# Kernel tuning notes

Measured on AMD Instinct MI355X. Metric: run time of the kernel, lower is better.

Reference implementation:

```python
import jax, jax.numpy as jnp
import numpy as np

P = 8          # patch_size
DIM = 256      # embed dim
HEADS = 8
HEAD_DIM = DIM // HEADS
CH = 3
PATCH_DIM = CH * P * P  # 192
INNER = int(4.0 * DIM)  # 1024
SCALE = HEAD_DIM ** -0.5


def sine_pos_embedding(n, c, dtype=jnp.float32):
    # standard 1D sinusoidal position encoding, shape (n, c)
    pos = jnp.arange(n, dtype=jnp.float32)[:, None]            # (n,1)
    div = jnp.exp(jnp.arange(0, c, 2, dtype=jnp.float32) * (-np.log(10000.0) / c))
    pe = jnp.zeros((n, c), dtype=jnp.float32)
    pe = pe.at[:, 0::2].set(jnp.sin(pos * div))
    pe = pe.at[:, 1::2].set(jnp.cos(pos * div))
    return pe.astype(dtype)


def patchify(x):
    # (B,C,H,W) -> (B, n, p1*p2*C), matching 'b c (h p1) (w p2) -> b (h w) (p1 p2 c)'
    B, C, H, W = x.shape
    hp, wp = H // P, W // P
    x = x.reshape(B, C, hp, P, wp, P)
    x = x.transpose(0, 2, 4, 3, 5, 1)        # (B, hp, wp, p1, p2, C)
    return x.reshape(B, hp * wp, P * P * C)


def unpatchify(x, hp, wp):
    # (B, n, p1*p2*C) -> (B, C, H, W)
    B = x.shape[0]
    x = x.reshape(B, hp, wp, P, P, CH)
    x = x.transpose(0, 5, 1, 3, 2, 4)        # (B, C, hp, p1, wp, p2)
    return x.reshape(B, CH, hp * P, wp * P)


def setup_inputs() -> dict:
    key = jax.random.key(0)
    ks = jax.random.split(key, 16)
    B, H, W = 8, 256, 256
    s = 0.02
    img0 = jax.random.normal(ks[0], (B, CH, H, W), dtype=jnp.float32)
    img1 = jax.random.normal(ks[1], (B, CH, H, W), dtype=jnp.float32)
    mask = jax.random.randint(ks[2], (B, 1, H, W), 0, 2).astype(jnp.float32)
    return {
        "img0": img0,
        "img1": img1,
        "mask": mask,
        "w_patch": jax.random.normal(ks[3], (PATCH_DIM, DIM), jnp.float32) * s,
        "b_patch": jnp.zeros((DIM,), jnp.float32),
        "w_kv": jax.random.normal(ks[4], (DIM, 2 * DIM), jnp.float32) * s,
        "b_kv": jnp.zeros((2 * DIM,), jnp.float32),
        "w_qv": jax.random.normal(ks[5], (DIM, 2 * DIM), jnp.float32) * s,
        "b_qv": jnp.zeros((2 * DIM,), jnp.float32),
        "w_fc1": jax.random.normal(ks[6], (DIM, INNER), jnp.float32) * s,
        "b_fc1": jnp.zeros((INNER,), jnp.float32),
        "w_fc2": jax.random.normal(ks[7], (INNER, PATCH_DIM), jnp.float32) * s,
        "b_fc2": jnp.zeros((PATCH_DIM,), jnp.float32),
    }


def reference(img0, img1, mask, w_patch, b_patch, w_kv, b_kv, w_qv, b_qv,
              w_fc1, b_fc1, w_fc2, b_fc2):
    B, C, H, W = img0.shape
    hp, wp = H // P, W // P
    n = hp * wp

    x0 = patchify(img0) @ w_patch + b_patch   # (B, n, dim)
    x1 = patchify(img1) @ w_patch + b_patch
    pe = sine_pos_embedding(n, DIM)
    x0 = x0 + pe
    x1 = x1 + pe

    # img0 -> k, v
    kv = (x0 @ w_kv + b_kv).reshape(B, n, 2, HEADS, HEAD_DIM)
    kv = kv.transpose(2, 0, 3, 1, 4)          # (2, B, heads, n, hd)
    k, v = kv[0], kv[1]

    # img1 -> q (v1 unused in forward, matching torch code)
    qv = (x1 @ w_qv + b_qv).reshape(B, n, 2, DIM).transpose(2, 0, 1, 3)
    q = qv[0].reshape(B, n, HEADS, HEAD_DIM).transpose(0, 2, 1, 3)  # (B, heads, n, hd)

    dots = jnp.einsum('bhqd,bhkd->bhqk', q, k) * SCALE  # (B, heads, n, n)

    # mask: (B,1,H,W) -> per-patch sum -> binary -> additive bias over key dim
    msum = mask.reshape(B, 1, hp, P, wp, P).sum(axis=(3, 5)).reshape(B, 1, n)
    bias = jnp.where(msum > 0, 0.0, -100.0)[:, :, None, :]  # (B,1,1,n)

    attn = jax.nn.softmax(dots + bias, axis=-1)
    out = jnp.einsum('bhqk,bhkd->bhqd', attn, v)
    out = out.transpose(0, 2, 1, 3).reshape(B, n, DIM)

    # mlp2: Linear -> GELU(exact) -> Linear
    h = jax.nn.gelu(out @ w_fc1 + b_fc1, approximate=False)
    res = h @ w_fc2 + b_fc2                   # (B, n, patch_dim)

    return unpatchify(res, hp, wp)            # (B, C, H, W)
```

## Files before the change

### kernel.cpp

```cpp
#include <hip/hip_runtime.h>
#include <cstdint>
#include <cstddef>

typedef __bf16 bf16_t;
typedef uint32_t u32;
typedef __bf16 bf16x4 __attribute__((ext_vector_type(4)));
typedef __bf16 bf16x8 __attribute__((ext_vector_type(8)));
typedef float f32x4 __attribute__((ext_vector_type(4)));
typedef float f32x16 __attribute__((ext_vector_type(16)));

__device__ __forceinline__ void gload_lds16(const bf16_t* g, bf16_t* l) {
  __builtin_amdgcn_global_load_lds((const __attribute__((address_space(1))) void*)g,
                                   (__attribute__((address_space(3))) void*)l,
                                   16, 0, 0);
}

__device__ __forceinline__ f32x4 mfma16(bf16x8 a, bf16x8 b, f32x4 c) {
  return __builtin_amdgcn_mfma_f32_16x16x32_bf16(a, b, c, 0, 0, 0);
}
__device__ __forceinline__ f32x16 mfma32(bf16x8 a, bf16x8 b, f32x16 c) {
  return __builtin_amdgcn_mfma_f32_32x32x16_bf16(a, b, c, 0, 0, 0);
}

#define LOG2E 1.4426950408889634f

__global__ __launch_bounds__(256)
void prep_all(const float* __restrict__ img0, const float* __restrict__ img1,
              const float* __restrict__ mask,
              const float* __restrict__ wp, const float* __restrict__ wkv,
              const float* __restrict__ wqv, const float* __restrict__ wfc1,
              const float* __restrict__ wfc2,
              bf16_t* __restrict__ xp0, bf16_t* __restrict__ xp1,
              float* __restrict__ pe, float* __restrict__ bias,
              bf16_t* __restrict__ wpT, bf16_t* __restrict__ wkvT,
              bf16_t* __restrict__ wqT, bf16_t* __restrict__ wfc1T,
              bf16_t* __restrict__ wfc2T) {
  __shared__ float tl[64 * 65];
  int bid = blockIdx.x, tid = threadIdx.x;
  if (bid < 1536) {
    int imgsel = bid >= 768;
    int t = (bid - (imgsel ? 768 : 0)) * 256 + tid;
    const float* img = imgsel ? img1 : img0;
    bf16_t* xp = imgsel ? xp1 : xp0;
    int wpp = t & 31, p1 = (t >> 5) & 7, hp = (t >> 8) & 31, rest = t >> 13;
    int b = rest / 3, c = rest - b * 3;
    const float* src = img + (((size_t)(b * 3 + c) * 256 + hp * 8 + p1) * 256 + wpp * 8);
    float4 v0 = *(const float4*)src;
    float4 v1 = *(const float4*)(src + 4);
    int row = b * 1024 + hp * 32 + wpp;
    bf16_t* dst = xp + (size_t)row * 192 + p1 * 24 + c;
    dst[0]  = (bf16_t)v0.x; dst[3]  = (bf16_t)v0.y; dst[6]  = (bf16_t)v0.z; dst[9]  = (bf16_t)v0.w;
    dst[12] = (bf16_t)v1.x; dst[15] = (bf16_t)v1.y; dst[18] = (bf16_t)v1.z; dst[21] = (bf16_t)v1.w;
  } else if (bid < 2560) {
    int t = bid - 1536, c = tid;
    int i2 = c & ~1;
    float div = __expf((float)i2 * (-9.210340371976184f / 256.0f));
    float arg = (float)t * div;
    float sv, cv;
    __sincosf(arg, &sv, &cv);
    pe[t * 256 + c] = (c & 1) ? cv : sv;
  } else if (bid < 2592) {
    int g = (bid - 2560) * 256 + tid;
    int b = g >> 10, t = g & 1023, hp = t >> 5, wpp = t & 31;
    const float* mp = mask + ((size_t)b * 256 + hp * 8) * 256 + wpp * 8;
    float s = 0.f;
    #pragma unroll
    for (int p1 = 0; p1 < 8; p1++) {
      float4 a = *(const float4*)(mp + p1 * 256);
      float4 c = *(const float4*)(mp + p1 * 256 + 4);
      s += a.x + a.y + a.z + a.w + c.x + c.y + c.z + c.w;
    }
    bias[g] = (s > 0.f) ? 0.f : (-100.f * LOG2E);
  } else {
    int i = bid - 2592;
    const float* src; bf16_t* dst; int srcN, dstK, NT;
    if (i >= 172) {
      int j = i - 172;
      bf16_t* p = wfc2T + 192 * 1024 + j * 8192 + tid * 32;
      bf16x8 z;
      #pragma unroll
      for (int e = 0; e < 8; e++) z[e] = (bf16_t)0.0f;
      *(bf16x8*)(p) = z; *(bf16x8*)(p + 8) = z;
      *(bf16x8*)(p + 16) = z; *(bf16x8*)(p + 24) = z;
      return;
    }
    if (i < 12)       { src = wp;   dst = wpT;   srcN = 256;  dstK = 192;  NT = 4; }
    else if (i < 44)  { i -= 12;  src = wkv;  dst = wkvT;  srcN = 512;  dstK = 256;  NT = 8; }
    else if (i < 60)  { i -= 44;  src = wqv;  dst = wqT;   srcN = 512;  dstK = 256;  NT = 4; }
    else if (i < 124) { i -= 60;  src = wfc1; dst = wfc1T; srcN = 1024; dstK = 256;  NT = 16; }
    else              { i -= 124; src = wfc2; dst = wfc2T; srcN = 192;  dstK = 1024; NT = 3; }
    int kt = i / NT, nt = i - kt * NT;
    #pragma unroll
    for (int j = 0; j < 4; j++) {
      int r = (tid >> 4) + 16 * j, c = (tid & 15) * 4;
      float4 v = *(const float4*)(src + (size_t)(kt * 64 + r) * srcN + nt * 64 + c);
      tl[r * 65 + c] = v.x; tl[r * 65 + c + 1] = v.y;
      tl[r * 65 + c + 2] = v.z; tl[r * 65 + c + 3] = v.w;
    }
    __syncthreads();
    #pragma unroll
    for (int j = 0; j < 16; j++) {
      int flat = tid + 256 * j;
      int n_l = flat >> 6, k_l = flat & 63;
      dst[(size_t)(nt * 64 + n_l) * dstK + kt * 64 + k_l] = (bf16_t)tl[k_l * 65 + n_l];
    }
  }
}

template<int EPI, int BN>
__global__ __launch_bounds__(256)
void gemm_bt(const bf16_t* __restrict__ A_, const bf16_t* __restrict__ A2,
             const bf16_t* __restrict__ Bt_, const bf16_t* __restrict__ Bt2,
             int M, int N, int K,
             const float* __restrict__ bias_, const float* __restrict__ bias2,
             const float* __restrict__ pe,
             bf16_t* __restrict__ out_b, bf16_t* __restrict__ out_b2,
             bf16_t* __restrict__ out_b3, float* __restrict__ out_f) {
  constexpr int NF = BN / 32;
  __shared__ bf16_t alds[2][8 * 64 * 8];
  __shared__ bf16_t blds[2][8 * BN * 8];
  const int tid = threadIdx.x;
  const int lane = tid & 63, wid = tid >> 6;
  const int ln15 = lane & 15, hi = lane >> 4;
  const int brow = blockIdx.x * 64;
  int bcol = blockIdx.y * BN;
  const bf16_t* A = A_;
  const bf16_t* Bt = Bt_;
  const float* bias = bias_;
  bool qpart = false;
  if (EPI == 0 && blockIdx.z) A = A2;
  if (EPI == 5 && blockIdx.y >= 4) {
    qpart = true; A = A2; Bt = Bt2; bias = bias2; bcol -= 512;
  }
  const int wr = wid >> 1, wc = wid & 1;

  auto stage = [&](int buf, int k0) {
    #pragma unroll
    for (int s = 0; s < 2; s++) {
      int c = tid + s * 256; int kb = c >> 6, row = c & 63;
      gload_lds16(A + (size_t)(brow + row) * K + k0 + kb * 8,
                  &alds[buf][(size_t)(s * 256 + wid * 64) * 8]);
    }
    #pragma unroll
    for (int s = 0; s < BN / 32; s++) {
      int c = tid + s * 256; int kb = c / BN, row = c & (BN - 1);
      gload_lds16(Bt + (size_t)(bcol + row) * K + k0 + kb * 8,
                  &blds[buf][(size_t)(s * 256 + wid * 64) * 8]);
    }
  };

  f32x4 acc[2][NF];
  #pragma unroll
  for (int m = 0; m < 2; m++)
    #pragma unroll
    for (int n = 0; n < NF; n++) acc[m][n] = (f32x4){0.f, 0.f, 0.f, 0.f};

  stage(0, 0);
  __syncthreads();
  int cur = 0;
  const int NT = K >> 6;
  for (int t = 0; t < NT; t++) {
    if (t + 1 < NT) stage(cur ^ 1, (t + 1) << 6);
    bf16x8 af[2][2], bfr[2][NF];
    #pragma unroll
    for (int kk = 0; kk < 2; kk++) {
      #pragma unroll
      for (int m = 0; m < 2; m++)
        af[kk][m] = *(const bf16x8*)&alds[cur][(size_t)((kk * 4 + hi) * 64 + wr * 32 + m * 16 + ln15) * 8];
      #pragma unroll
      for (int n = 0; n < NF; n++)
        bfr[kk][n] = *(const bf16x8*)&blds[cur][(size_t)((kk * 4 + hi) * BN + wc * (BN / 2) + n * 16 + ln15) * 8];
    }
    #pragma unroll
    for (int kk = 0; kk < 2; kk++)
      #pragma unroll
      for (int m = 0; m < 2; m++)
        #pragma unroll
        for (int n = 0; n < NF; n++)
          acc[m][n] = mfma16(af[kk][m], bfr[kk][n], acc[m][n]);
    __syncthreads();
    cur ^= 1;
  }

  #pragma unroll
  for (int m = 0; m < 2; m++) {
    #pragma unroll
    for (int n = 0; n < NF; n++) {
      #pragma unroll
      for (int r = 0; r < 4; r++) {
        int grow = brow + wr * 32 + m * 16 + hi * 4 + r;
        int gcol = bcol + wc * (BN / 2) + n * 16 + ln15;
        float v = acc[m][n][r];
        if (EPI == 0) {
          v += bias[gcol] + pe[(grow & 1023) * 256 + gcol];
          bf16_t* outx = blockIdx.z ? out_b2 : out_b;
          outx[(size_t)grow * N + gcol] = (bf16_t)v;
        } else if (EPI == 5) {
          v += bias[gcol];
          int b = grow >> 10, t = grow & 1023;
          if (!qpart) {
            if (gcol < 256) {
              int h = gcol >> 5, d = gcol & 31;
              out_b[(((size_t)(b * 8 + h) * 1024 + t) << 5) + d] = (bf16_t)v;
            } else {
              int c2 = gcol - 256; int h = c2 >> 5, d = c2 & 31;
              out_b2[(((size_t)(b * 8 + h) * 32 + d) << 10) + t] = (bf16_t)v;
            }
          } else {
            v *= (0.17677669529663687f * LOG2E);
            int h = gcol >> 5, d = gcol & 31;
            out_b3[(((size_t)(b * 8 + h) * 1024 + t) << 5) + d] = (bf16_t)v;
          }
        } else if (EPI == 3) {
          v += bias[gcol];
          float gg = 0.5f * v * (1.0f + erff(v * 0.7071067811865476f));
          out_b[(size_t)grow * N + gcol] = (bf16_t)gg;
        } else if (EPI == 4) {
          if (gcol < 192) {
            v += bias[gcol];
            int b = grow >> 10, t = grow & 1023;
            int hp = t >> 5, wpp = t & 31;
            int p = gcol / 3; int c = gcol - p * 3;
            int p1 = p >> 3, p2 = p & 7;
            out_f[(((size_t)(b * 3 + c) * 256 + hp * 8 + p1) * 256) + wpp * 8 + p2] = v;
          }
        }
      }
    }
  }
}

union PW { u32 w[4]; bf16x8 v; };

__device__ __forceinline__ u32 pkbf(float a, float b) {
  union { bf16_t h[2]; u32 w; } u;
  u.h[0] = (bf16_t)a; u.h[1] = (bf16_t)b;
  return u.w;
}

__device__ __forceinline__ void pl32swap(u32& a, u32& b) {
  asm volatile("v_permlane32_swap_b32 %0, %1" : "+v"(a), "+v"(b));
}

#define SMEM_BYTES 32768

__device__ __forceinline__ void stage_kv(const bf16_t* kbase, const bf16_t* vbase,
                                         int ch, char* smem, int cur,
                                         int tid, int wid) {
  bf16_t* kl = (bf16_t*)(smem + cur * 8192);
  bf16_t* vl = (bf16_t*)(smem + 16384 + cur * 8192);
  #pragma unroll
  for (int s = 0; s < 2; s++) {
    int c = tid + s * 256;
    int row = c >> 2, cs = (c & 3) ^ (row & 3);
    gload_lds16(kbase + (size_t)(ch * 128 + row) * 32 + cs * 8,
                kl + (size_t)(s * 256 + wid * 64) * 8);
  }
  #pragma unroll
  for (int s = 0; s < 2; s++) {
    int c = tid + s * 256;
    int row = c >> 4, cs = (c & 15) ^ (row & 15);
    gload_lds16(vbase + (size_t)row * 1024 + ch * 128 + cs * 8,
                vl + (size_t)(s * 256 + wid * 64) * 8);
  }
}

__global__ __launch_bounds__(256, 4)
void attn_kernel(const bf16_t* __restrict__ q, const bf16_t* __restrict__ k,
                 const bf16_t* __restrict__ vt, const float* __restrict__ bias,
                 bf16_t* __restrict__ out) {
  __shared__ __align__(16) char smem[SMEM_BYTES];

  int tid = threadIdx.x, lane = tid & 63, wid = tid >> 6;
  int l31 = lane & 31, g = lane >> 5;
  int x = blockIdx.x & 7, idx = blockIdx.x >> 3;
  int qt = idx & 31;
  int bh = ((idx >> 5) << 3) | x;
  int b = bh >> 3, h = bh & 7;
  int q0 = qt * 32;
  const bf16_t* qp = q + ((size_t)bh * 1024 + q0 + l31) * 32;
  bf16x8 qf0 = *(const bf16x8*)(qp + g * 8);
  bf16x8 qf1 = *(const bf16x8*)(qp + 16 + g * 8);
  const bf16_t* kbase = k + (size_t)bh * 32768;
  const bf16_t* vbase = vt + (size_t)bh * 32768;
  const float* bb = bias + b * 1024;

  f32x16 acc;
  #pragma unroll
  for (int r = 0; r < 16; r++) acc[r] = 0.f;
  float lsum = 0.f;

  stage_kv(kbase, vbase, 0, smem, 0, tid, wid);
  __syncthreads();

  int cur = 0;
  for (int ch = 0; ch < 8; ch++) {
    if (ch < 7) stage_kv(kbase, vbase, ch + 1, smem, cur ^ 1, tid, wid);
    const bf16_t* kl = (const bf16_t*)(smem + cur * 8192);
    const bf16_t* vl = (const bf16_t*)(smem + 16384 + cur * 8192);
    int base = ch * 128 + wid * 32;
    int row0 = wid * 32 + l31;
    bf16x8 kA = *(const bf16x8*)(kl + (size_t)(row0 * 4 + (g ^ (row0 & 3))) * 8);
    bf16x8 kB = *(const bf16x8*)(kl + (size_t)(row0 * 4 + ((2 + g) ^ (row0 & 3))) * 8);
    bf16x8 vA = *(const bf16x8*)(vl + (size_t)(l31 * 16 + ((wid * 4 + g) ^ (l31 & 15))) * 8);
    bf16x8 vB = *(const bf16x8*)(vl + (size_t)(l31 * 16 + ((wid * 4 + 2 + g) ^ (l31 & 15))) * 8);
    f32x4 c0 = *(const f32x4*)(bb + base + 4 * g);
    f32x4 c1 = *(const f32x4*)(bb + base + 8 + 4 * g);
    f32x4 c2 = *(const f32x4*)(bb + base + 16 + 4 * g);
    f32x4 c3 = *(const f32x4*)(bb + base + 24 + 4 * g);
    f32x16 S;
    S[0] = c0[0]; S[1] = c0[1]; S[2] = c0[2]; S[3] = c0[3];
    S[4] = c1[0]; S[5] = c1[1]; S[6] = c1[2]; S[7] = c1[3];
    S[8] = c2[0]; S[9] = c2[1]; S[10] = c2[2]; S[11] = c2[3];
    S[12] = c3[0]; S[13] = c3[1]; S[14] = c3[2]; S[15] = c3[3];
    S = mfma32(kA, qf0, S);
    S = mfma32(kB, qf1, S);
    float p[16];
    #pragma unroll
    for (int r = 0; r < 16; r++) p[r] = exp2f(S[r]);
    lsum += (((p[0] + p[1]) + (p[2] + p[3])) + ((p[4] + p[5]) + (p[6] + p[7]))) +
            (((p[8] + p[9]) + (p[10] + p[11])) + ((p[12] + p[13]) + (p[14] + p[15])));
    u32 w[8];
    #pragma unroll
    for (int j = 0; j < 8; j++) w[j] = pkbf(p[2 * j], p[2 * j + 1]);
    u32 xa = w[2], ya = w[0]; pl32swap(xa, ya);
    u32 xb = w[3], yb = w[1]; pl32swap(xb, yb);
    u32 xc = w[6], yc = w[4]; pl32swap(xc, yc);
    u32 xd = w[7], yd = w[5]; pl32swap(xd, yd);
    PW A0, A1;
    A0.w[0] = g ? xa : w[0];  A0.w[2] = g ? w[2] : ya;
    A0.w[1] = g ? xb : w[1];  A0.w[3] = g ? w[3] : yb;
    A1.w[0] = g ? xc : w[4];  A1.w[2] = g ? w[6] : yc;
    A1.w[1] = g ? xd : w[5];  A1.w[3] = g ? w[7] : yd;
    acc = mfma32(A0.v, vA, acc);
    acc = mfma32(A1.v, vB, acc);
    __syncthreads();
    cur ^= 1;
  }

  float* OL = (float*)smem;
  float* LS = (float*)(smem + 16896);
  #pragma unroll
  for (int r = 0; r < 16; r++) {
    int row = (r & 3) + 8 * (r >> 2) + 4 * g;
    OL[wid * 1056 + row * 33 + l31] = acc[r];
  }
  lsum += __shfl_xor(lsum, 32);
  LS[wid * 32 + l31] = lsum;
  __syncthreads();

  int qq = tid >> 3, d0 = (tid & 7) * 4;
  float l = LS[qq] + LS[32 + qq] + LS[64 + qq] + LS[96 + qq];
  float o0 = 0.f, o1 = 0.f, o2 = 0.f, o3 = 0.f;
  #pragma unroll
  for (int w2 = 0; w2 < 4; w2++) {
    const float* p = &OL[w2 * 1056 + qq * 33 + d0];
    o0 += p[0]; o1 += p[1]; o2 += p[2]; o3 += p[3];
  }
  float linv = 1.f / l;
  bf16x4 ov;
  ov[0] = (bf16_t)(o0 * linv); ov[1] = (bf16_t)(o1 * linv);
  ov[2] = (bf16_t)(o2 * linv); ov[3] = (bf16_t)(o3 * linv);
  *(bf16x4*)(out + ((size_t)b * 1024 + q0 + qq) * 256 + h * 32 + d0) = ov;
}

extern "C" void kernel_launch(void* const* d_in, const int* in_sizes, int n_in,
                              void* d_out, int out_size, void* d_ws, size_t ws_size,
                              hipStream_t stream) {
  (void)in_sizes; (void)n_in; (void)out_size; (void)ws_size;
  const float* img0    = (const float*)d_in[0];
  const float* img1    = (const float*)d_in[1];
  const float* mask    = (const float*)d_in[2];
  const float* w_patch = (const float*)d_in[3];
  const float* b_patch = (const float*)d_in[4];
  const float* w_kv    = (const float*)d_in[5];
  const float* b_kv    = (const float*)d_in[6];
  const float* w_qv    = (const float*)d_in[7];
  const float* b_qv    = (const float*)d_in[8];
  const float* w_fc1   = (const float*)d_in[9];
  const float* b_fc1   = (const float*)d_in[10];
  const float* w_fc2   = (const float*)d_in[11];
  const float* b_fc2   = (const float*)d_in[12];
  float* out = (float*)d_out;

  char* ws = (char*)d_ws;
  float*  pe    = (float*)(ws + 0);
  float*  bias  = (float*)(ws + 1048576);
  bf16_t* wpT   = (bf16_t*)(ws + 1081344);
  bf16_t* wkvT  = (bf16_t*)(ws + 1179648);
  bf16_t* wqT   = (bf16_t*)(ws + 1441792);
  bf16_t* wfc1T = (bf16_t*)(ws + 1572864);
  bf16_t* wfc2T = (bf16_t*)(ws + 2097152);
  bf16_t* xp0   = (bf16_t*)(ws + 2621440);
  bf16_t* xp1   = (bf16_t*)(ws + 5767168);
  bf16_t* x0    = (bf16_t*)(ws + 8912896);
  bf16_t* x1    = (bf16_t*)(ws + 13107200);
  bf16_t* kbuf  = (bf16_t*)(ws + 17301504);
  bf16_t* vtbuf = (bf16_t*)(ws + 21495808);
  bf16_t* qbuf  = (bf16_t*)(ws + 25690112);
  bf16_t* aout  = (bf16_t*)(ws + 29884416);
  bf16_t* hbuf  = (bf16_t*)(ws + 34078720);

  prep_all<<<2772, 256, 0, stream>>>(img0, img1, mask, w_patch, w_kv, w_qv, w_fc1, w_fc2,
                                     xp0, xp1, pe, bias, wpT, wkvT, wqT, wfc1T, wfc2T);

  gemm_bt<0, 128><<<dim3(128, 2, 2), 256, 0, stream>>>(xp0, xp1, wpT, nullptr, 8192, 256, 192,
                                                       b_patch, nullptr, pe, x0, x1, nullptr, nullptr);
  gemm_bt<5, 128><<<dim3(128, 6), 256, 0, stream>>>(x0, x1, wkvT, wqT, 8192, 512, 256,
                                                    b_kv, b_qv, nullptr, kbuf, vtbuf, qbuf, nullptr);

  attn_kernel<<<2048, 256, 0, stream>>>(qbuf, kbuf, vtbuf, bias, aout);

  gemm_bt<3, 128><<<dim3(128, 8), 256, 0, stream>>>(aout, nullptr, wfc1T, nullptr, 8192, 1024, 256,
                                                    b_fc1, nullptr, nullptr, hbuf, nullptr, nullptr, nullptr);
  gemm_bt<4, 64><<<dim3(128, 4), 256, 0, stream>>>(hbuf, nullptr, wfc2T, nullptr, 8192, 256, 1024,
                                                   b_fc2, nullptr, nullptr, nullptr, nullptr, nullptr, out);
}
```

Before: 117.7 us.

## Use 128-row GEMM tiles with single-buffered K=32 steps, split fc2 kernel

The patch-embed, kv/q projection and fc1 GEMMs now use 128-row M tiles with four 16-row fragments per wave, and stage K in steps of 32 through one LDS buffer. This raises data reuse per tile and halves the block count. It drops the double-buffered prefetch, so each step now waits on its loads between two barriers. fc2 moves into its own kernel that keeps the old 64-row double-buffered scheme and launches only 3 column tiles, so no blocks are spent on the padded columns beyond 192.

```diff
diff --git a/kernel.cpp b/kernel.cpp
--- a/kernel.cpp
+++ b/kernel.cpp
@@ -109,7 +109,7 @@
 
 template<int EPI, int BN>
 __global__ __launch_bounds__(256)
-void gemm_bt(const bf16_t* __restrict__ A_, const bf16_t* __restrict__ A2,
+void gemm128(const bf16_t* __restrict__ A_, const bf16_t* __restrict__ A2,
              const bf16_t* __restrict__ Bt_, const bf16_t* __restrict__ Bt2,
              int M, int N, int K,
              const float* __restrict__ bias_, const float* __restrict__ bias2,
@@ -117,12 +117,12 @@
              bf16_t* __restrict__ out_b, bf16_t* __restrict__ out_b2,
              bf16_t* __restrict__ out_b3, float* __restrict__ out_f) {
   constexpr int NF = BN / 32;
-  __shared__ bf16_t alds[2][8 * 64 * 8];
-  __shared__ bf16_t blds[2][8 * BN * 8];
+  __shared__ bf16_t alds[4 * 128 * 8];
+  __shared__ bf16_t blds[4 * BN * 8];
   const int tid = threadIdx.x;
   const int lane = tid & 63, wid = tid >> 6;
   const int ln15 = lane & 15, hi = lane >> 4;
-  const int brow = blockIdx.x * 64;
+  const int brow = blockIdx.x * 128;
   int bcol = blockIdx.y * BN;
   const bf16_t* A = A_;
   const bf16_t* Bt = Bt_;
@@ -134,61 +134,48 @@
   }
   const int wr = wid >> 1, wc = wid & 1;
 
-  auto stage = [&](int buf, int k0) {
+  f32x4 acc[4][NF];
+  #pragma unroll
+  for (int m = 0; m < 4; m++)
+    #pragma unroll
+    for (int n = 0; n < NF; n++) acc[m][n] = (f32x4){0.f, 0.f, 0.f, 0.f};
+
+  for (int k0 = 0; k0 < K; k0 += 32) {
     #pragma unroll
     for (int s = 0; s < 2; s++) {
-      int c = tid + s * 256; int kb = c >> 6, row = c & 63;
+      int c = tid + s * 256; int kb = c >> 7, row = c & 127;
       gload_lds16(A + (size_t)(brow + row) * K + k0 + kb * 8,
-                  &alds[buf][(size_t)(s * 256 + wid * 64) * 8]);
-    }
-    #pragma unroll
-    for (int s = 0; s < BN / 32; s++) {
-      int c = tid + s * 256; int kb = c / BN, row = c & (BN - 1);
+                  &alds[(size_t)(s * 256 + wid * 64) * 8]);
+    }
+    #pragma unroll
+    for (int s = 0; s < BN / 64; s++) {
+      int c = tid + s * 256; int kb = c / BN, row = c % BN;
       gload_lds16(Bt + (size_t)(bcol + row) * K + k0 + kb * 8,
-                  &blds[buf][(size_t)(s * 256 + wid * 64) * 8]);
-    }
-  };
-
-  f32x4 acc[2][NF];
-  #pragma unroll
-  for (int m = 0; m < 2; m++)
-    #pragma unroll
-    for (int n = 0; n < NF; n++) acc[m][n] = (f32x4){0.f, 0.f, 0.f, 0.f};
-
-  stage(0, 0);
-  __syncthreads();
-  int cur = 0;
-  const int NT = K >> 6;
-  for (int t = 0; t < NT; t++) {
-    if (t + 1 < NT) stage(cur ^ 1, (t + 1) << 6);
-    bf16x8 af[2][2], bfr[2][NF];
-    #pragma unroll
-    for (int kk = 0; kk < 2; kk++) {
-      #pragma unroll
-      for (int m = 0; m < 2; m++)
-        af[kk][m] = *(const bf16x8*)&alds[cur][(size_t)((kk * 4 + hi) * 64 + wr * 32 + m * 16 + ln15) * 8];
+                  &blds[(size_t)(s * 256 + wid * 64) * 8]);
+    }
+    __syncthreads();
+    bf16x8 af[4], bfr[NF];
+    #pragma unroll
+    for (int m = 0; m < 4; m++)
+      af[m] = *(const bf16x8*)&alds[(size_t)(hi * 128 + wr * 64 + m * 16 + ln15) * 8];
+    #pragma unroll
+    for (int n = 0; n < NF; n++)
+      bfr[n] = *(const bf16x8*)&blds[(size_t)(hi * BN + wc * (BN / 2) + n * 16 + ln15) * 8];
+    #pragma unroll
+    for (int m = 0; m < 4; m++)
       #pragma unroll
       for (int n = 0; n < NF; n++)
-        bfr[kk][n] = *(const bf16x8*)&blds[cur][(size_t)((kk * 4 + hi) * BN + wc * (BN / 2) + n * 16 + ln15) * 8];
-    }
-    #pragma unroll
-    for (int kk = 0; kk < 2; kk++)
-      #pragma unroll
-      for (int m = 0; m < 2; m++)
-        #pragma unroll
-        for (int n = 0; n < NF; n++)
-          acc[m][n] = mfma16(af[kk][m], bfr[kk][n], acc[m][n]);
+        acc[m][n] = mfma16(af[m], bfr[n], acc[m][n]);
     __syncthreads();
-    cur ^= 1;
-  }
-
-  #pragma unroll
-  for (int m = 0; m < 2; m++) {
+  }
+
+  #pragma unroll
+  for (int m = 0; m < 4; m++) {
     #pragma unroll
     for (int n = 0; n < NF; n++) {
       #pragma unroll
       for (int r = 0; r < 4; r++) {
-        int grow = brow + wr * 32 + m * 16 + hi * 4 + r;
+        int grow = brow + wr * 64 + m * 16 + hi * 4 + r;
         int gcol = bcol + wc * (BN / 2) + n * 16 + ln15;
         float v = acc[m][n][r];
         if (EPI == 0) {
@@ -215,16 +202,89 @@
           v += bias[gcol];
           float gg = 0.5f * v * (1.0f + erff(v * 0.7071067811865476f));
           out_b[(size_t)grow * N + gcol] = (bf16_t)gg;
-        } else if (EPI == 4) {
-          if (gcol < 192) {
-            v += bias[gcol];
-            int b = grow >> 10, t = grow & 1023;
-            int hp = t >> 5, wpp = t & 31;
-            int p = gcol / 3; int c = gcol - p * 3;
-            int p1 = p >> 3, p2 = p & 7;
-            out_f[(((size_t)(b * 3 + c) * 256 + hp * 8 + p1) * 256) + wpp * 8 + p2] = v;
-          }
         }
+      }
+    }
+  }
+}
+
+template<int BN>
+__global__ __launch_bounds__(256)
+void gemm_fc2(const bf16_t* __restrict__ A, const bf16_t* __restrict__ Bt,
+              int M, int N, int K, const float* __restrict__ bias,
+              float* __restrict__ out_f) {
+  constexpr int NF = BN / 32;
+  __shared__ bf16_t alds[2][8 * 64 * 8];
+  __shared__ bf16_t blds[2][8 * BN * 8];
+  const int tid = threadIdx.x;
+  const int lane = tid & 63, wid = tid >> 6;
+  const int ln15 = lane & 15, hi = lane >> 4;
+  const int brow = blockIdx.x * 64;
+  const int bcol = blockIdx.y * BN;
+  const int wr = wid >> 1, wc = wid & 1;
+
+  auto stage = [&](int buf, int k0) {
+    #pragma unroll
+    for (int s = 0; s < 2; s++) {
+      int c = tid + s * 256; int kb = c >> 6, row = c & 63;
+      gload_lds16(A + (size_t)(brow + row) * K + k0 + kb * 8,
+                  &alds[buf][(size_t)(s * 256 + wid * 64) * 8]);
+    }
+    #pragma unroll
+    for (int s = 0; s < BN / 32; s++) {
+      int c = tid + s * 256; int kb = c / BN, row = c & (BN - 1);
+      gload_lds16(Bt + (size_t)(bcol + row) * K + k0 + kb * 8,
+                  &blds[buf][(size_t)(s * 256 + wid * 64) * 8]);
+    }
+  };
+
+  f32x4 acc[2][NF];
+  #pragma unroll
+  for (int m = 0; m < 2; m++)
+    #pragma unroll
+    for (int n = 0; n < NF; n++) acc[m][n] = (f32x4){0.f, 0.f, 0.f, 0.f};
+
+  stage(0, 0);
+  __syncthreads();
+  int cur = 0;
+  const int NT = K >> 6;
+  for (int t = 0; t < NT; t++) {
+    if (t + 1 < NT) stage(cur ^ 1, (t + 1) << 6);
+    bf16x8 af[2][2], bfr[2][NF];
+    #pragma unroll
+    for (int kk = 0; kk < 2; kk++) {
+      #pragma unroll
+      for (int m = 0; m < 2; m++)
+        af[kk][m] = *(const bf16x8*)&alds[cur][(size_t)((kk * 4 + hi) * 64 + wr * 32 + m * 16 + ln15) * 8];
+      #pragma unroll
+      for (int n = 0; n < NF; n++)
+        bfr[kk][n] = *(const bf16x8*)&blds[cur][(size_t)((kk * 4 + hi) * BN + wc * (BN / 2) + n * 16 + ln15) * 8];
+    }
+    #pragma unroll
+    for (int kk = 0; kk < 2; kk++)
+      #pragma unroll
+      for (int m = 0; m < 2; m++)
+        #pragma unroll
+        for (int n = 0; n < NF; n++)
+          acc[m][n] = mfma16(af[kk][m], bfr[kk][n], acc[m][n]);
+    __syncthreads();
+    cur ^= 1;
+  }
+
+  #pragma unroll
+  for (int m = 0; m < 2; m++) {
+    #pragma unroll
+    for (int n = 0; n < NF; n++) {
+      #pragma unroll
+      for (int r = 0; r < 4; r++) {
+        int grow = brow + wr * 32 + m * 16 + hi * 4 + r;
+        int gcol = bcol + wc * (BN / 2) + n * 16 + ln15;
+        float v = acc[m][n][r] + bias[gcol];
+        int b = grow >> 10, t = grow & 1023;
+        int hp = t >> 5, wpp = t & 31;
+        int p = gcol / 3; int c = gcol - p * 3;
+        int p1 = p >> 3, p2 = p & 7;
+        out_f[(((size_t)(b * 3 + c) * 256 + hp * 8 + p1) * 256) + wpp * 8 + p2] = v;
       }
     }
   }
@@ -404,15 +464,14 @@
   prep_all<<<2772, 256, 0, stream>>>(img0, img1, mask, w_patch, w_kv, w_qv, w_fc1, w_fc2,
                                      xp0, xp1, pe, bias, wpT, wkvT, wqT, wfc1T, wfc2T);
 
-  gemm_bt<0, 128><<<dim3(128, 2, 2), 256, 0, stream>>>(xp0, xp1, wpT, nullptr, 8192, 256, 192,
-                                                       b_patch, nullptr, pe, x0, x1, nullptr, nullptr);
-  gemm_bt<5, 128><<<dim3(128, 6), 256, 0, stream>>>(x0, x1, wkvT, wqT, 8192, 512, 256,
-                                                    b_kv, b_qv, nullptr, kbuf, vtbuf, qbuf, nullptr);
+  gemm128<0, 64><<<dim3(64, 4, 2), 256, 0, stream>>>(xp0, xp1, wpT, nullptr, 8192, 256, 192,
+                                                     b_patch, nullptr, pe, x0, x1, nullptr, nullptr);
+  gemm128<5, 128><<<dim3(64, 6), 256, 0, stream>>>(x0, x1, wkvT, wqT, 8192, 512, 256,
+                                                   b_kv, b_qv, nullptr, kbuf, vtbuf, qbuf, nullptr);
 
   attn_kernel<<<2048, 256, 0, stream>>>(qbuf, kbuf, vtbuf, bias, aout);
 
-  gemm_bt<3, 128><<<dim3(128, 8), 256, 0, stream>>>(aout, nullptr, wfc1T, nullptr, 8192, 1024, 256,
-                                                    b_fc1, nullptr, nullptr, hbuf, nullptr, nullptr, nullptr);
-  gemm_bt<4, 64><<<dim3(128, 4), 256, 0, stream>>>(hbuf, nullptr, wfc2T, nullptr, 8192, 256, 1024,
-                                                   b_fc2, nullptr, nullptr, nullptr, nullptr, nullptr, out);
-}
+  gemm128<3, 128><<<dim3(64, 8), 256, 0, stream>>>(aout, nullptr, wfc1T, nullptr, 8192, 1024, 256,
+                                                   b_fc1, nullptr, nullptr, hbuf, nullptr, nullptr, nullptr);
+  gemm_fc2<64><<<dim3(128, 3), 256, 0, stream>>>(hbuf, wfc2T, 8192, 256, 1024, b_fc2, out);
+}
```

Result: no change. 117.5 us (-0.1%).

## Replace double-buffered GEMM with single-buffered 64x64 tile GEMM using K-step 32

Applied to the files above, without the earlier changes.

Swaps the templated BN-wide, double-buffered GEMM (K-step 64) for a fixed 64x64 tile kernel that stages one K=32 slice per iteration into a single LDS buffer and syncs twice per step. Launch bounds now request 4 blocks per CU, and grids are widened so more, smaller blocks cover each GEMM. The fc2 grid shrinks to exactly the 192 valid columns, which removes the column guard. The aim is more occupancy and less wasted work on the padded fc2 columns. The cost is losing load/compute overlap, paying twice as many barriers and less operand reuse per tile.

```diff
diff --git a/kernel.cpp b/kernel.cpp
--- a/kernel.cpp
+++ b/kernel.cpp
@@ -107,89 +107,68 @@
   }
 }
 
-template<int EPI, int BN>
-__global__ __launch_bounds__(256)
-void gemm_bt(const bf16_t* __restrict__ A_, const bf16_t* __restrict__ A2,
-             const bf16_t* __restrict__ Bt_, const bf16_t* __restrict__ Bt2,
-             int M, int N, int K,
-             const float* __restrict__ bias_, const float* __restrict__ bias2,
-             const float* __restrict__ pe,
-             bf16_t* __restrict__ out_b, bf16_t* __restrict__ out_b2,
-             bf16_t* __restrict__ out_b3, float* __restrict__ out_f) {
-  constexpr int NF = BN / 32;
-  __shared__ bf16_t alds[2][8 * 64 * 8];
-  __shared__ bf16_t blds[2][8 * BN * 8];
+template<int EPI>
+__global__ __launch_bounds__(256, 4)
+void gemm64(const bf16_t* __restrict__ A_, const bf16_t* __restrict__ A2,
+            const bf16_t* __restrict__ Bt_, const bf16_t* __restrict__ Bt2,
+            int M, int N, int K,
+            const float* __restrict__ bias_, const float* __restrict__ bias2,
+            const float* __restrict__ pe,
+            bf16_t* __restrict__ out_b, bf16_t* __restrict__ out_b2,
+            bf16_t* __restrict__ out_b3, float* __restrict__ out_f) {
+  __shared__ bf16_t alds[4 * 64 * 8];
+  __shared__ bf16_t blds[4 * 64 * 8];
   const int tid = threadIdx.x;
   const int lane = tid & 63, wid = tid >> 6;
   const int ln15 = lane & 15, hi = lane >> 4;
   const int brow = blockIdx.x * 64;
-  int bcol = blockIdx.y * BN;
+  int bcol = blockIdx.y * 64;
   const bf16_t* A = A_;
   const bf16_t* Bt = Bt_;
   const float* bias = bias_;
   bool qpart = false;
   if (EPI == 0 && blockIdx.z) A = A2;
-  if (EPI == 5 && blockIdx.y >= 4) {
+  if (EPI == 5 && blockIdx.y >= 8) {
     qpart = true; A = A2; Bt = Bt2; bias = bias2; bcol -= 512;
   }
   const int wr = wid >> 1, wc = wid & 1;
-
-  auto stage = [&](int buf, int k0) {
-    #pragma unroll
-    for (int s = 0; s < 2; s++) {
-      int c = tid + s * 256; int kb = c >> 6, row = c & 63;
-      gload_lds16(A + (size_t)(brow + row) * K + k0 + kb * 8,
-                  &alds[buf][(size_t)(s * 256 + wid * 64) * 8]);
-    }
-    #pragma unroll
-    for (int s = 0; s < BN / 32; s++) {
-      int c = tid + s * 256; int kb = c / BN, row = c & (BN - 1);
-      gload_lds16(Bt + (size_t)(bcol + row) * K + k0 + kb * 8,
-                  &blds[buf][(size_t)(s * 256 + wid * 64) * 8]);
-    }
-  };
-
-  f32x4 acc[2][NF];
+  const int arow = tid & 63, akb = tid >> 6;
+
+  f32x4 acc[2][2];
   #pragma unroll
   for (int m = 0; m < 2; m++)
     #pragma unroll
-    for (int n = 0; n < NF; n++) acc[m][n] = (f32x4){0.f, 0.f, 0.f, 0.f};
-
-  stage(0, 0);
-  __syncthreads();
-  int cur = 0;
-  const int NT = K >> 6;
-  for (int t = 0; t < NT; t++) {
-    if (t + 1 < NT) stage(cur ^ 1, (t + 1) << 6);
-    bf16x8 af[2][2], bfr[2][NF];
-    #pragma unroll
-    for (int kk = 0; kk < 2; kk++) {
+    for (int n = 0; n < 2; n++) acc[m][n] = (f32x4){0.f, 0.f, 0.f, 0.f};
+
+  for (int k0 = 0; k0 < K; k0 += 32) {
+    gload_lds16(A + (size_t)(brow + arow) * K + k0 + akb * 8,
+                alds + (size_t)(wid * 64) * 8);
+    gload_lds16(Bt + (size_t)(bcol + arow) * K + k0 + akb * 8,
+                blds + (size_t)(wid * 64) * 8);
+    __syncthreads();
+    bf16x8 af[2], bf[2];
+    #pragma unroll
+    for (int m = 0; m < 2; m++)
+      af[m] = *(const bf16x8*)&alds[(size_t)(hi * 64 + wr * 32 + m * 16 + ln15) * 8];
+    #pragma unroll
+    for (int n = 0; n < 2; n++)
+      bf[n] = *(const bf16x8*)&blds[(size_t)(hi * 64 + wc * 32 + n * 16 + ln15) * 8];
+    #pragma unroll
+    for (int m = 0; m < 2; m++)
       #pragma unroll
-      for (int m = 0; m < 2; m++)
-        af[kk][m] = *(const bf16x8*)&alds[cur][(size_t)((kk * 4 + hi) * 64 + wr * 32 + m * 16 + ln15) * 8];
-      #pragma unroll
-      for (int n = 0; n < NF; n++)
-        bfr[kk][n] = *(const bf16x8*)&blds[cur][(size_t)((kk * 4 + hi) * BN + wc * (BN / 2) + n * 16 + ln15) * 8];
-    }
-    #pragma unroll
-    for (int kk = 0; kk < 2; kk++)
-      #pragma unroll
-      for (int m = 0; m < 2; m++)
-        #pragma unroll
-        for (int n = 0; n < NF; n++)
-          acc[m][n] = mfma16(af[kk][m], bfr[kk][n], acc[m][n]);
+      for (int n = 0; n < 2; n++)
+        acc[m][n] = mfma16(af[m], bf[n], acc[m][n]);
     __syncthreads();
-    cur ^= 1;
   }
 
   #pragma unroll
   for (int m = 0; m < 2; m++) {
     #pragma unroll
-    for (int n = 0; n < NF; n++) {
+    for (int n = 0; n < 2; n++) {
       #pragma unroll
       for (int r = 0; r < 4; r++) {
         int grow = brow + wr * 32 + m * 16 + hi * 4 + r;
-        int gcol = bcol + wc * (BN / 2) + n * 16 + ln15;
+        int gcol = bcol + wc * 32 + n * 16 + ln15;
         float v = acc[m][n][r];
         if (EPI == 0) {
           v += bias[gcol] + pe[(grow & 1023) * 256 + gcol];
@@ -216,14 +195,12 @@
           float gg = 0.5f * v * (1.0f + erff(v * 0.7071067811865476f));
           out_b[(size_t)grow * N + gcol] = (bf16_t)gg;
         } else if (EPI == 4) {
-          if (gcol < 192) {
-            v += bias[gcol];
-            int b = grow >> 10, t = grow & 1023;
-            int hp = t >> 5, wpp = t & 31;
-            int p = gcol / 3; int c = gcol - p * 3;
-            int p1 = p >> 3, p2 = p & 7;
-            out_f[(((size_t)(b * 3 + c) * 256 + hp * 8 + p1) * 256) + wpp * 8 + p2] = v;
-          }
+          v += bias[gcol];
+          int b = grow >> 10, t = grow & 1023;
+          int hp = t >> 5, wpp = t & 31;
+          int p = gcol / 3; int c = gcol - p * 3;
+          int p1 = p >> 3, p2 = p & 7;
+          out_f[(((size_t)(b * 3 + c) * 256 + hp * 8 + p1) * 256) + wpp * 8 + p2] = v;
         }
       }
     }
@@ -404,15 +381,15 @@
   prep_all<<<2772, 256, 0, stream>>>(img0, img1, mask, w_patch, w_kv, w_qv, w_fc1, w_fc2,
                                      xp0, xp1, pe, bias, wpT, wkvT, wqT, wfc1T, wfc2T);
 
-  gemm_bt<0, 128><<<dim3(128, 2, 2), 256, 0, stream>>>(xp0, xp1, wpT, nullptr, 8192, 256, 192,
-                                                       b_patch, nullptr, pe, x0, x1, nullptr, nullptr);
-  gemm_bt<5, 128><<<dim3(128, 6), 256, 0, stream>>>(x0, x1, wkvT, wqT, 8192, 512, 256,
-                                                    b_kv, b_qv, nullptr, kbuf, vtbuf, qbuf, nullptr);
+  gemm64<0><<<dim3(128, 4, 2), 256, 0, stream>>>(xp0, xp1, wpT, nullptr, 8192, 256, 192,
+                                                 b_patch, nullptr, pe, x0, x1, nullptr, nullptr);
+  gemm64<5><<<dim3(128, 12), 256, 0, stream>>>(x0, x1, wkvT, wqT, 8192, 512, 256,
+                                               b_kv, b_qv, nullptr, kbuf, vtbuf, qbuf, nullptr);
 
   attn_kernel<<<2048, 256, 0, stream>>>(qbuf, kbuf, vtbuf, bias, aout);
 
-  gemm_bt<3, 128><<<dim3(128, 8), 256, 0, stream>>>(aout, nullptr, wfc1T, nullptr, 8192, 1024, 256,
-                                                    b_fc1, nullptr, nullptr, hbuf, nullptr, nullptr, nullptr);
-  gemm_bt<4, 64><<<dim3(128, 4), 256, 0, stream>>>(hbuf, nullptr, wfc2T, nullptr, 8192, 256, 1024,
-                                                   b_fc2, nullptr, nullptr, nullptr, nullptr, nullptr, out);
-}
+  gemm64<3><<<dim3(128, 16), 256, 0, stream>>>(aout, nullptr, wfc1T, nullptr, 8192, 1024, 256,
+                                               b_fc1, nullptr, nullptr, hbuf, nullptr, nullptr, nullptr);
+  gemm64<4><<<dim3(128, 3), 256, 0, stream>>>(hbuf, nullptr, wfc2T, nullptr, 8192, 256, 1024,
+                                              b_fc2, nullptr, nullptr, nullptr, nullptr, nullptr, out);
+}
```

Result: slower. 123.7 us (+5.1%).
